# Kernel tuning notes

Hardware: AMD Instinct MI355X
Metric: run time of the kernel (lower is better)

Reference implementation:

```python
import jax, jax.numpy as jnp
import numpy as np

K = 20
EPS = 1e-5
DILATIONS = (1, 2, 4)


def _bn(x, g, b, m, v):
    # inference-mode BatchNorm1d (eval: running stats)
    return (x - m) / jnp.sqrt(v + EPS) * g + b


def _dilated_adj(x, dilation, k):
    B, N, _ = x.shape
    sq = jnp.sum(x * x, axis=-1)
    # squared pairwise distance: monotonic in p=2 cdist -> identical topk indices
    dist2 = sq[:, :, None] + sq[:, None, :] - 2.0 * jnp.einsum('bnc,bmc->bnm', x, x)
    dk = min(k * dilation, N - 1)
    _, idx = jax.lax.top_k(-dist2, dk + 1)          # smallest distances
    sampled = idx[:, :, 1::dilation][:, :, :k]      # skip self, dilated sample (B,N,k)
    bidx = jnp.arange(B)[:, None, None]
    ridx = jnp.arange(N)[None, :, None]
    return jnp.zeros((B, N, N), x.dtype).at[bidx, ridx, sampled].set(1.0)


def _normalize(adj):
    # add self loops then symmetric normalization D^-1/2 (A+I) D^-1/2
    N = adj.shape[1]
    a = adj + jnp.eye(N, dtype=adj.dtype)
    dinv = 1.0 / jnp.sqrt(jnp.sum(a, axis=2))       # degrees >= 1, no inf
    return dinv[:, :, None] * a * dinv[:, None, :]


def _gcn_layer(x, adj, W, b, g, bb, m, v):
    h = x @ W + b                                   # (B,N,Cout)
    h = jnp.einsum('bnm,bmc->bnc', adj, h)          # dense aggregation (bmm)
    return jax.nn.relu(_bn(h, g, bb, m, v))         # dropout is identity in eval


def _forward(x, Wg0, bg0, g0g, g0b, g0m, g0v, Wg1, bg1, g1g, g1b, g1m, g1v, Wg2, bg2, g2g, g2b, g2m, g2v, W1, b1, n1g, n1b, n1m, n1v, W2, b2, n2g, n2b, n2m, n2v, W3, b3, n3g, n3b, n3m, n3v, W4, b4, n4g, n4b, n4m, n4v, W5, b5, n5g, n5b, n5m, n5v, W6, b6):
    gcn_params = ((Wg0, bg0, g0g, g0b, g0m, g0v),
                  (Wg1, bg1, g1g, g1b, g1m, g1v),
                  (Wg2, bg2, g2g, g2b, g2m, g2v))
    feats = x
    ms = []
    for (W, b, g, bb, m, v), dil in zip(gcn_params, DILATIONS):
        adj = _normalize(_dilated_adj(feats, dil, K))
        feats = _gcn_layer(feats, adj, W, b, g, bb, m, v)
        ms.append(feats)
    f = jnp.stack(ms, axis=-1).mean(axis=-1)        # multi-scale mean (B,N,64)
    f = jax.nn.relu(_bn(f @ W1 + b1, n1g, n1b, n1m, n1v))
    f = jax.nn.relu(_bn(f @ W2 + b2, n2g, n2b, n2m, n2v))
    f = jax.nn.relu(_bn(f @ W3 + b3, n3g, n3b, n3m, n3v))
    f = jnp.max(f, axis=1)                          # MaxPool1d(N) over points -> (B,1024)
    f = jax.nn.relu(_bn(f @ W4 + b4, n4g, n4b, n4m, n4v))
    f = jax.nn.relu(_bn(f @ W5 + b5, n5g, n5b, n5m, n5v))
    return f @ W6 + b6                              # (B,40)


def setup_inputs():
    key = jax.random.key(0)
    ks = iter(jax.random.split(key, 32))
    d = {'x': jax.random.normal(next(ks), (32, 1024, 3), jnp.float32)}

    def lin(wn, bn_, ci, co):
        d[wn] = jax.random.normal(next(ks), (ci, co), jnp.float32) * 0.05
        d[bn_] = jnp.zeros((co,), jnp.float32)

    def bnp(p, c):
        d[p + 'g'] = jnp.ones((c,), jnp.float32)
        d[p + 'b'] = jnp.zeros((c,), jnp.float32)
        d[p + 'm'] = jnp.zeros((c,), jnp.float32)
        d[p + 'v'] = jnp.ones((c,), jnp.float32)

    for i, (ci, co) in enumerate(((3, 64), (64, 64), (64, 64))):
        lin('Wg%d' % i, 'bg%d' % i, ci, co)
        bnp('g%d' % i, co)
    for i, (ci, co) in enumerate(((64, 128), (128, 512), (512, 1024), (1024, 1024), (1024, 512)), start=1):
        lin('W%d' % i, 'b%d' % i, ci, co)
        bnp('n%d' % i, co)
    lin('W6', 'b6', 512, 40)
    return d


def reference(x, Wg0, bg0, g0g, g0b, g0m, g0v, Wg1, bg1, g1g, g1b, g1m, g1v, Wg2, bg2, g2g, g2b, g2m, g2v, W1, b1, n1g, n1b, n1m, n1v, W2, b2, n2g, n2b, n2m, n2v, W3, b3, n3g, n3b, n3m, n3v, W4, b4, n4g, n4b, n4m, n4v, W5, b5, n5g, n5b, n5m, n5v, W6, b6):
    return _forward(x, Wg0, bg0, g0g, g0b, g0m, g0v, Wg1, bg1, g1g, g1b, g1m, g1v, Wg2, bg2, g2g, g2b, g2m, g2v, W1, b1, n1g, n1b, n1m, n1v, W2, b2, n2g, n2b, n2m, n2v, W3, b3, n3g, n3b, n3m, n3v, W4, b4, n4g, n4b, n4m, n4v, W5, b5, n5g, n5b, n5m, n5v, W6, b6)
```

## Files before the change

kernel.cpp:

```cpp
#include <hip/hip_runtime.h>
#include <stdint.h>

#define KNN_K 20
#define EPSBN 1e-5f

typedef __attribute__((ext_vector_type(4))) float f32x4;
typedef __attribute__((ext_vector_type(8))) short s16x8;
typedef __attribute__((ext_vector_type(4))) short s16x4;

__device__ __forceinline__ unsigned sortable_f32(float f) {
    unsigned u = __float_as_uint(f);
    return (u & 0x80000000u) ? ~u : (u | 0x80000000u);
}

__device__ __forceinline__ short f2bf(float x) {
    unsigned u = __float_as_uint(x);
    unsigned r = (u + 0x7fffu + ((u >> 16) & 1u)) >> 16;
    return (short)r;
}
__device__ __forceinline__ float bf2f(short h) {
    return __uint_as_float(((unsigned)(unsigned short)h) << 16);
}

__global__ void sq_kernel(const float* __restrict__ x, float* __restrict__ sq,
                          int total, int C) {
    int i = blockIdx.x * 256 + threadIdx.x;
    if (i >= total) return;
    const float* p = x + (size_t)i * C;
    float s = 0.f;
    for (int c = 0; c < C; ++c) s += p[c] * p[c];
    sq[i] = s;
}

__global__ __launch_bounds__(256) void dist128_kernel(
    const float* __restrict__ feats, const float* __restrict__ sq,
    float* __restrict__ dist, int b0, int N, int C)
{
    int lb = blockIdx.z;
    int b = b0 + lb;
    const float* F = feats + (size_t)b * N * C;
    const float* S = sq + (size_t)b * N;
    float* D = dist + (size_t)lb * N * N;
    int n0 = blockIdx.y * 128, m0 = blockIdx.x * 128;
    __shared__ float As[16][132];
    __shared__ float Bs[16][132];
    int tx = threadIdx.x & 15, ty = threadIdx.x >> 4;
    int tid = threadIdx.x;
    float acc[8][8] = {};
    for (int k0 = 0; k0 < C; k0 += 16) {
        #pragma unroll
        for (int it = 0; it < 8; ++it) {
            int idx = tid + it * 256;
            int r = idx >> 4, kk = idx & 15;
            int gk = k0 + kk;
            As[kk][r] = (gk < C) ? F[(size_t)(n0 + r) * C + gk] : 0.f;
            Bs[kk][r] = (gk < C) ? F[(size_t)(m0 + r) * C + gk] : 0.f;
        }
        __syncthreads();
        #pragma unroll
        for (int kk = 0; kk < 16; ++kk) {
            float4 a0 = *reinterpret_cast<const float4*>(&As[kk][ty * 4]);
            float4 a1 = *reinterpret_cast<const float4*>(&As[kk][64 + ty * 4]);
            float4 b0 = *reinterpret_cast<const float4*>(&Bs[kk][tx * 4]);
            float4 b1 = *reinterpret_cast<const float4*>(&Bs[kk][64 + tx * 4]);
            float av[8] = {a0.x, a0.y, a0.z, a0.w, a1.x, a1.y, a1.z, a1.w};
            float bv[8] = {b0.x, b0.y, b0.z, b0.w, b1.x, b1.y, b1.z, b1.w};
            #pragma unroll
            for (int i = 0; i < 8; ++i)
                #pragma unroll
                for (int j = 0; j < 8; ++j)
                    acc[i][j] = fmaf(av[i], bv[j], acc[i][j]);
        }
        __syncthreads();
    }
    #pragma unroll
    for (int i = 0; i < 8; ++i) {
        int n = n0 + ((i < 4) ? ty * 4 + i : 64 + ty * 4 + (i - 4));
        float sn = S[n];
        #pragma unroll
        for (int j = 0; j < 8; ++j) {
            int m = m0 + ((j < 4) ? tx * 4 + j : 64 + tx * 4 + (j - 4));
            D[(size_t)n * N + m] = (sn + S[m]) - 2.0f * acc[i][j];
        }
    }
}

__global__ __launch_bounds__(256) void knn_agg_kernel(
    const float* __restrict__ dist, const float* __restrict__ lin,
    const float* __restrict__ gam, const float* __restrict__ bet,
    const float* __restrict__ mu, const float* __restrict__ var,
    float* __restrict__ feats_out, float* __restrict__ ms,
    short* __restrict__ msh, short* __restrict__ msl,
    int b0, int N, int dil, int mode)
{
    __shared__ unsigned long long keys[1024];
    __shared__ unsigned hist[2048];
    __shared__ unsigned long long cand[256];
    __shared__ int nbrs[KNN_K];
    __shared__ float aggP[4][64];
    __shared__ int wsum[4];
    __shared__ int svC0, svP, svD, svCounter;

    int t = threadIdx.x;
    int lb = blockIdx.x / N;
    int n = blockIdx.x - lb * N;
    int b = b0 + lb;
    const int R = KNN_K * dil + 1;

    const float* drow = dist + ((size_t)lb * N + n) * N;
    unsigned long long myk[4];
    #pragma unroll
    for (int s = 0; s < 4; ++s) {
        int m = t + 256 * s;
        float dv = drow[m];
        myk[s] = ((unsigned long long)sortable_f32(dv) << 32) | (unsigned)m;
        keys[m] = myk[s];
    }
    #pragma unroll
    for (int h = 0; h < 8; ++h) hist[t * 8 + h] = 0u;
    if (t == 0) svCounter = 0;
    __syncthreads();
    #pragma unroll
    for (int s = 0; s < 4; ++s)
        atomicAdd(&hist[(unsigned)(myk[s] >> 53)], 1u);
    __syncthreads();
    int psum = 0;
    #pragma unroll
    for (int h = 0; h < 8; ++h) psum += (int)hist[t * 8 + h];
    int lane = t & 63, wv = t >> 6;
    int val = psum;
    #pragma unroll
    for (int d = 1; d < 64; d <<= 1) {
        int o = __shfl_up(val, d, 64);
        if (lane >= d) val += o;
    }
    if (lane == 63) wsum[wv] = val;
    __syncthreads();
    int prefix = 0;
    for (int i = 0; i < wv; ++i) prefix += wsum[i];
    int incl = val + prefix;
    int excl = incl - psum;
    if (excl < R && incl >= R) {
        int cum = excl;
        for (int h = 0; h < 8; ++h) {
            int hv = (int)hist[t * 8 + h];
            if (cum + hv >= R) { svD = t * 8 + h; svC0 = cum; svP = hv; break; }
            cum += hv;
        }
    }
    __syncthreads();
    int Cnt = svC0 + svP;
    if (Cnt <= 256) {
        unsigned dpiv = (unsigned)svD;
        #pragma unroll
        for (int s = 0; s < 4; ++s) {
            if ((unsigned)(myk[s] >> 53) <= dpiv) {
                int pos = atomicAdd(&svCounter, 1);
                cand[pos] = myk[s];
            }
        }
        __syncthreads();
        if (t < Cnt) {
            unsigned long long my = cand[t];
            int r = 0;
            for (int c = 0; c < Cnt; ++c) r += (cand[c] < my) ? 1 : 0;
            if (r >= 1) {
                int q = r - 1;
                if (q % dil == 0) {
                    int j = q / dil;
                    if (j < KNN_K) nbrs[j] = (int)(my & 0xFFFFFFFFull);
                }
            }
        }
        __syncthreads();
    } else {
        for (int kk = 2; kk <= 1024; kk <<= 1) {
            for (int jj = kk >> 1; jj > 0; jj >>= 1) {
                __syncthreads();
                #pragma unroll
                for (int s = 0; s < 4; ++s) {
                    int i = t + 256 * s;
                    int ixj = i ^ jj;
                    if (ixj > i) {
                        unsigned long long a = keys[i], c = keys[ixj];
                        bool up = ((i & kk) == 0);
                        if ((a > c) == up) { keys[i] = c; keys[ixj] = a; }
                    }
                }
            }
        }
        __syncthreads();
        if (t < KNN_K) nbrs[t] = (int)(keys[1 + t * dil] & 0xFFFFFFFFull);
        __syncthreads();
    }
    {
        int c = t & 63, g = t >> 6;
        float pacc = 0.f;
        for (int j = g; j < KNN_K; j += 4)
            pacc += lin[((size_t)b * N + nbrs[j]) * 64 + c];
        aggP[g][c] = pacc;
    }
    __syncthreads();
    if (t < 64) {
        const float sc = 1.0f / 21.0f;
        size_t base = ((size_t)b * N + n) * 64;
        float acc = lin[base + t] + aggP[0][t] + aggP[1][t] + aggP[2][t] + aggP[3][t];
        float v = acc * sc;
        v = (v - mu[t]) / sqrtf(var[t] + EPSBN) * gam[t] + bet[t];
        v = fmaxf(v, 0.f);
        if (feats_out) feats_out[base + t] = v;
        if (mode == 0) ms[base + t] = v;
        else if (mode == 1) ms[base + t] += v;
        else {
            float m3 = (ms[base + t] + v) * (1.0f / 3.0f);
            short hh = f2bf(m3);
            msh[base + t] = hh;
            msl[base + t] = f2bf(m3 - bf2f(hh));
        }
    }
}

template<int EPI>
__global__ __launch_bounds__(256) void gemm_kernel(
    const float* __restrict__ A, const float* __restrict__ W,
    const float* __restrict__ bias,
    const float* __restrict__ gam, const float* __restrict__ bet,
    const float* __restrict__ mu, const float* __restrict__ var,
    float* __restrict__ C,
    int M, int K, int N)
{
    __shared__ float As[16][68];
    __shared__ float Bs[16][68];
    int tx = threadIdx.x, ty = threadIdx.y;
    int tid = ty * 16 + tx;
    int row0 = blockIdx.y * 64, col0 = blockIdx.x * 64;
    float acc[4][4] = {};
    for (int k0 = 0; k0 < K; k0 += 16) {
        #pragma unroll
        for (int it = 0; it < 4; ++it) {
            int idx = tid + it * 256;
            int r = idx >> 4, kk = idx & 15;
            int gr = row0 + r, gk = k0 + kk;
            As[kk][r] = (gr < M && gk < K) ? A[(size_t)gr * K + gk] : 0.f;
        }
        #pragma unroll
        for (int it = 0; it < 4; ++it) {
            int idx = tid + it * 256;
            int kk = idx >> 6, c = idx & 63;
            int gk = k0 + kk, gc = col0 + c;
            Bs[kk][c] = (gk < K && gc < N) ? W[(size_t)gk * N + gc] : 0.f;
        }
        __syncthreads();
        #pragma unroll
        for (int kk = 0; kk < 16; ++kk) {
            float4 a4 = *reinterpret_cast<const float4*>(&As[kk][ty * 4]);
            float4 b4 = *reinterpret_cast<const float4*>(&Bs[kk][tx * 4]);
            float av[4] = {a4.x, a4.y, a4.z, a4.w};
            float bv[4] = {b4.x, b4.y, b4.z, b4.w};
            #pragma unroll
            for (int i = 0; i < 4; ++i)
                #pragma unroll
                for (int j = 0; j < 4; ++j)
                    acc[i][j] = fmaf(av[i], bv[j], acc[i][j]);
        }
        __syncthreads();
    }
    #pragma unroll
    for (int i = 0; i < 4; ++i) {
        int r = row0 + ty * 4 + i;
        if (r >= M) break;
        #pragma unroll
        for (int j = 0; j < 4; ++j) {
            int c = col0 + tx * 4 + j;
            if (c >= N) continue;
            float val = acc[i][j] + bias[c];
            if (EPI >= 1) {
                val = (val - mu[c]) / sqrtf(var[c] + EPSBN) * gam[c] + bet[c];
                val = fmaxf(val, 0.f);
            }
            C[(size_t)r * N + c] = val;
        }
    }
}

__global__ __launch_bounds__(256) void skinny_gemm_kernel(
    const float* __restrict__ A, const float* __restrict__ W,
    float* __restrict__ part, int K, int N)
{
    __shared__ float Alds[32][260];
    int tid = threadIdx.x;
    int col0 = blockIdx.x * 32;
    int kc = blockIdx.y;
    int k0 = kc * 256;
    #pragma unroll
    for (int it = 0; it < 8; ++it) {
        int idx = tid + it * 256;
        int r = idx >> 6, kq = (idx & 63) * 4;
        f32x4 v = *(const f32x4*)&A[(size_t)r * K + k0 + kq];
        *(f32x4*)&Alds[r][kq] = v;
    }
    __syncthreads();

    int col = col0 + (tid & 31);
    int g = tid >> 5;
    bool colok = col < N;
    const float* Wp = W + (size_t)k0 * N + (colok ? col : 0);
    float acc0 = 0.f, acc1 = 0.f, acc2 = 0.f, acc3 = 0.f;
    #pragma unroll 4
    for (int k = 0; k < 256; ++k) {
        float wv = Wp[(size_t)k * N];
        acc0 = fmaf(Alds[g * 4 + 0][k], wv, acc0);
        acc1 = fmaf(Alds[g * 4 + 1][k], wv, acc1);
        acc2 = fmaf(Alds[g * 4 + 2][k], wv, acc2);
        acc3 = fmaf(Alds[g * 4 + 3][k], wv, acc3);
    }
    if (colok) {
        size_t base = ((size_t)kc * 32 + g * 4) * N + col;
        part[base]         = acc0;
        part[base + N]     = acc1;
        part[base + 2 * N] = acc2;
        part[base + 3 * N] = acc3;
    }
}

template<int EPI>
__global__ void skinny_reduce_kernel(
    const float* __restrict__ part, const float* __restrict__ bias,
    const float* __restrict__ gam, const float* __restrict__ bet,
    const float* __restrict__ mu, const float* __restrict__ var,
    float* __restrict__ C, int M, int N, int kchunks)
{
    int i = blockIdx.x * 256 + threadIdx.x;
    if (i >= M * N) return;
    int c = i % N;
    float s = 0.f;
    for (int kc = 0; kc < kchunks; ++kc) s += part[(size_t)kc * M * N + i];
    float val = s + bias[c];
    if (EPI >= 1) {
        val = (val - mu[c]) / sqrtf(var[c] + EPSBN) * gam[c] + bet[c];
        val = fmaxf(val, 0.f);
    }
    C[i] = val;
}

__global__ void split_wt_kernel(const float* __restrict__ W,
                                short* __restrict__ Bh, short* __restrict__ Bl,
                                int K, int N)
{
    int n = blockIdx.x * 64 + threadIdx.x;
    if (n >= N) return;
    for (int k0 = 0; k0 < K; k0 += 8) {
        s16x8 h, l;
        #pragma unroll
        for (int e = 0; e < 8; ++e) {
            float x = W[(size_t)(k0 + e) * N + n];
            short hh = f2bf(x);
            h[e] = hh;
            l[e] = f2bf(x - bf2f(hh));
        }
        *(s16x8*)&Bh[(size_t)n * K + k0] = h;
        *(s16x8*)&Bl[(size_t)n * K + k0] = l;
    }
}

template<int EPI>
__global__ __launch_bounds__(256) void gemm_mfma_kernel(
    const short* __restrict__ Ah, const short* __restrict__ Al,
    const short* __restrict__ Bh, const short* __restrict__ Bl,
    const float* __restrict__ bias,
    const float* __restrict__ gam, const float* __restrict__ bet,
    const float* __restrict__ mu, const float* __restrict__ var,
    short* __restrict__ Chi, short* __restrict__ Clo,
    float* __restrict__ pool,
    int M, int K, int N, int rowsPerBatch)
{
    __shared__ short Alds[128][72];
    __shared__ short Blds[128][72];
    __shared__ int poolS[128];

    int tid = threadIdx.x;
    int wave = tid >> 6, lane = tid & 63;
    int wr = wave >> 1, wc = wave & 1;
    int row0 = blockIdx.y * 128, col0 = blockIdx.x * 128;
    int fr = lane & 15, fq = lane >> 4;
    int kb = fq * 8;

    f32x4 acc[4][4] = {};

    for (int k0 = 0; k0 < K; k0 += 32) {
        #pragma unroll
        for (int it = 0; it < 2; ++it) {
            int idx = tid + it * 256;
            int r = idx >> 2, ch = (idx & 3) * 8;
            size_t go = (size_t)(row0 + r) * K + k0 + ch;
            *(s16x8*)&Alds[r][ch]      = *(const s16x8*)&Ah[go];
            *(s16x8*)&Alds[r][32 + ch] = *(const s16x8*)&Al[go];
        }
        #pragma unroll
        for (int it = 0; it < 2; ++it) {
            int idx = tid + it * 256;
            int c = idx >> 2, ch = (idx & 3) * 8;
            size_t bo = (size_t)(col0 + c) * K + k0 + ch;
            *(s16x8*)&Blds[c][ch]      = *(const s16x8*)&Bh[bo];
            *(s16x8*)&Blds[c][32 + ch] = *(const s16x8*)&Bl[bo];
        }
        __syncthreads();

        s16x8 ah[4], al[4], bhf[4], blf[4];
        #pragma unroll
        for (int i = 0; i < 4; ++i) {
            int r = wr * 64 + i * 16 + fr;
            ah[i] = *(const s16x8*)&Alds[r][kb];
            al[i] = *(const s16x8*)&Alds[r][32 + kb];
        }
        #pragma unroll
        for (int j = 0; j < 4; ++j) {
            int c = wc * 64 + j * 16 + fr;
            bhf[j] = *(const s16x8*)&Blds[c][kb];
            blf[j] = *(const s16x8*)&Blds[c][32 + kb];
        }
        #pragma unroll
        for (int i = 0; i < 4; ++i)
            #pragma unroll
            for (int j = 0; j < 4; ++j) {
                acc[i][j] = __builtin_amdgcn_mfma_f32_16x16x32_bf16(ah[i], bhf[j], acc[i][j], 0, 0, 0);
                acc[i][j] = __builtin_amdgcn_mfma_f32_16x16x32_bf16(ah[i], blf[j], acc[i][j], 0, 0, 0);
                acc[i][j] = __builtin_amdgcn_mfma_f32_16x16x32_bf16(al[i], bhf[j], acc[i][j], 0, 0, 0);
            }
        __syncthreads();
    }

    if (EPI == 1) {
        #pragma unroll
        for (int j = 0; j < 4; ++j) {
            int col = col0 + wc * 64 + j * 16 + fr;
            float bs = bias[col], g = gam[col], be = bet[col], m = mu[col];
            float inv = 1.0f / sqrtf(var[col] + EPSBN);
            #pragma unroll
            for (int i = 0; i < 4; ++i) {
                int rbase = row0 + wr * 64 + i * 16 + fq * 4;
                #pragma unroll
                for (int reg = 0; reg < 4; ++reg) {
                    float val = acc[i][j][reg] + bs;
                    val = (val - m) * inv * g + be;
                    val = fmaxf(val, 0.f);
                    short hh = f2bf(val);
                    size_t o = (size_t)(rbase + reg) * N + col;
                    Chi[o] = hh;
                    Clo[o] = f2bf(val - bf2f(hh));
                }
            }
        }
    } else {
        float cmax[4];
        #pragma unroll
        for (int j = 0; j < 4; ++j) {
            int col = col0 + wc * 64 + j * 16 + fr;
            float bs = bias[col], g = gam[col], be = bet[col], m = mu[col];
            float inv = 1.0f / sqrtf(var[col] + EPSBN);
            float cm = 0.f;
            #pragma unroll
            for (int i = 0; i < 4; ++i)
                #pragma unroll
                for (int reg = 0; reg < 4; ++reg) {
                    float val = acc[i][j][reg] + bs;
                    val = (val - m) * inv * g + be;
                    val = fmaxf(val, 0.f);
                    cm = fmaxf(cm, val);
                }
            cmax[j] = cm;
        }
        #pragma unroll
        for (int j = 0; j < 4; ++j) {
            cmax[j] = fmaxf(cmax[j], __shfl_xor(cmax[j], 16, 64));
            cmax[j] = fmaxf(cmax[j], __shfl_xor(cmax[j], 32, 64));
        }
        if (tid < 128) poolS[tid] = 0;
        __syncthreads();
        if (fq == 0) {
            #pragma unroll
            for (int j = 0; j < 4; ++j)
                atomicMax(&poolS[wc * 64 + j * 16 + fr], __float_as_int(cmax[j]));
        }
        __syncthreads();
        if (tid < 128) {
            int bb = row0 / rowsPerBatch;
            atomicMax((int*)&pool[(size_t)bb * N + col0 + tid], poolS[tid]);
        }
    }
}

extern "C" void kernel_launch(void* const* d_in, const int* in_sizes, int n_in,
                              void* d_out, int out_size, void* d_ws, size_t ws_size,
                              hipStream_t stream)
{
    (void)in_sizes; (void)n_in; (void)out_size;
    const int B = 32, N = 1024, MBN = B * N;
    const float* x = (const float*)d_in[0];

    const float *Wg[3], *bg[3], *gg[3], *gb[3], *gm[3], *gv[3];
    for (int i = 0; i < 3; ++i) {
        int base = 1 + i * 6;
        Wg[i] = (const float*)d_in[base + 0];
        bg[i] = (const float*)d_in[base + 1];
        gg[i] = (const float*)d_in[base + 2];
        gb[i] = (const float*)d_in[base + 3];
        gm[i] = (const float*)d_in[base + 4];
        gv[i] = (const float*)d_in[base + 5];
    }
    const float *Wm[5], *bm[5], *ng[5], *nb[5], *nm[5], *nv[5];
    for (int i = 0; i < 5; ++i) {
        int base = 19 + i * 6;
        Wm[i] = (const float*)d_in[base + 0];
        bm[i] = (const float*)d_in[base + 1];
        ng[i] = (const float*)d_in[base + 2];
        nb[i] = (const float*)d_in[base + 3];
        nm[i] = (const float*)d_in[base + 4];
        nv[i] = (const float*)d_in[base + 5];
    }
    const float* W6 = (const float*)d_in[49];
    const float* b6 = (const float*)d_in[50];

    char* w = (char*)d_ws;
    size_t off = 0;
    auto allocB = [&](size_t bytes) {
        void* p = w + off;
        off += (bytes + 255) & ~(size_t)255;
        return p;
    };
    float* ms     = (float*)allocB((size_t)MBN * 64 * 4);
    float* fA     = (float*)allocB((size_t)MBN * 64 * 4);
    float* fB     = (float*)allocB((size_t)MBN * 64 * 4);
    float* lin    = (float*)allocB((size_t)MBN * 64 * 4);
    float* sqv    = (float*)allocB((size_t)MBN * 4);
    float* pooled = (float*)allocB((size_t)B * 1024 * 4);
    float* f4     = (float*)allocB((size_t)B * 1024 * 4);
    float* f5     = (float*)allocB((size_t)B * 512 * 4);
    float* skpart = (float*)allocB((size_t)4 * 32 * 1024 * 4);
    short* msh    = (short*)allocB((size_t)MBN * 64 * 2);
    short* msl    = (short*)allocB((size_t)MBN * 64 * 2);
    short* w1h    = (short*)allocB((size_t)64 * 128 * 2);
    short* w1l    = (short*)allocB((size_t)64 * 128 * 2);
    short* w2h    = (short*)allocB((size_t)128 * 512 * 2);
    short* w2l    = (short*)allocB((size_t)128 * 512 * 2);
    short* w3h    = (short*)allocB((size_t)512 * 1024 * 2);
    short* w3l    = (short*)allocB((size_t)512 * 1024 * 2);
    size_t bigOff = off;
    short* f1h = (short*)(w + bigOff);
    short* f1l = (short*)(w + bigOff + 1 * (size_t)MBN * 128 * 2);
    short* f2h = (short*)(w + bigOff + 2 * (size_t)MBN * 128 * 2);
    short* f2l = (short*)(w + bigOff + 2 * (size_t)MBN * 128 * 2 + (size_t)MBN * 512 * 2);
    float* distB = (float*)(w + bigOff);
    size_t distBytes = (size_t)N * N * sizeof(float);
    int chunkB = 1;
    if (ws_size > bigOff) {
        size_t cap = (ws_size - bigOff) / distBytes;
        chunkB = (int)(cap < 32 ? cap : 32);
        if (chunkB < 1) chunkB = 1;
    }

    dim3 blk16(16, 16);
    auto grid64  = [](int M, int Nn) { return dim3((unsigned)((Nn + 63) / 64), (unsigned)((M + 63) / 64)); };
    auto gridMf  = [](int M, int Nn) { return dim3((unsigned)(Nn / 128), (unsigned)(M / 128)); };

    split_wt_kernel<<<dim3(128 / 64), 64, 0, stream>>>(Wm[0], w1h, w1l, 64, 128);
    split_wt_kernel<<<dim3(512 / 64), 64, 0, stream>>>(Wm[1], w2h, w2l, 128, 512);
    split_wt_kernel<<<dim3(1024 / 64), 64, 0, stream>>>(Wm[2], w3h, w3l, 512, 1024);

    const float* featsIn = x;
    float* featsOutArr[3] = { fA, fB, nullptr };
    int Cin[3] = { 3, 64, 64 };
    int dils[3] = { 1, 2, 4 };
    for (int L = 0; L < 3; ++L) {
        sq_kernel<<<(MBN + 255) / 256, 256, 0, stream>>>(featsIn, sqv, MBN, Cin[L]);
        gemm_kernel<0><<<grid64(MBN, 64), blk16, 0, stream>>>(
            featsIn, Wg[L], bg[L], nullptr, nullptr, nullptr, nullptr,
            lin, MBN, Cin[L], 64);
        for (int b0 = 0; b0 < B; b0 += chunkB) {
            int cb = (B - b0 < chunkB) ? (B - b0) : chunkB;
            dist128_kernel<<<dim3(8, 8, (unsigned)cb), 256, 0, stream>>>(
                featsIn, sqv, distB, b0, N, Cin[L]);
            knn_agg_kernel<<<cb * N, 256, 0, stream>>>(
                distB, lin, gg[L], gb[L], gm[L], gv[L],
                featsOutArr[L], ms, msh, msl, b0, N, dils[L], L);
        }
        featsIn = featsOutArr[L];
    }

    gemm_mfma_kernel<1><<<gridMf(MBN, 128), 256, 0, stream>>>(
        msh, msl, w1h, w1l, bm[0], ng[0], nb[0], nm[0], nv[0],
        f1h, f1l, nullptr, MBN, 64, 128, N);
    gemm_mfma_kernel<1><<<gridMf(MBN, 512), 256, 0, stream>>>(
        f1h, f1l, w2h, w2l, bm[1], ng[1], nb[1], nm[1], nv[1],
        f2h, f2l, nullptr, MBN, 128, 512, N);
    hipMemsetAsync(pooled, 0, (size_t)B * 1024 * sizeof(float), stream);
    gemm_mfma_kernel<2><<<gridMf(MBN, 1024), 256, 0, stream>>>(
        f2h, f2l, w3h, w3l, bm[2], ng[2], nb[2], nm[2], nv[2],
        nullptr, nullptr, pooled, MBN, 512, 1024, N);

    skinny_gemm_kernel<<<dim3(1024 / 32, 4), 256, 0, stream>>>(pooled, Wm[3], skpart, 1024, 1024);
    skinny_reduce_kernel<1><<<(32 * 1024 + 255) / 256, 256, 0, stream>>>(
        skpart, bm[3], ng[3], nb[3], nm[3], nv[3], f4, 32, 1024, 4);
    skinny_gemm_kernel<<<dim3(512 / 32, 4), 256, 0, stream>>>(f4, Wm[4], skpart, 1024, 512);
    skinny_reduce_kernel<1><<<(32 * 512 + 255) / 256, 256, 0, stream>>>(
        skpart, bm[4], ng[4], nb[4], nm[4], nv[4], f5, 32, 512, 4);
    skinny_gemm_kernel<<<dim3(2, 2), 256, 0, stream>>>(f5, W6, skpart, 512, 40);
    skinny_reduce_kernel<0><<<(32 * 40 + 255) / 256, 256, 0, stream>>>(
        skpart, b6, nullptr, nullptr, nullptr, nullptr, (float*)d_out, 32, 40, 2);
}
```

Baseline: 817.2 us.

## Exploit distance symmetry, alias sort keys onto histogram LDS, XCD-aware GEMM tile mapping

The distance kernel now computes only upper-triangular 128x128 tiles (36 instead of 64) and writes each off-diagonal tile twice, once transposed, so the pairwise GEMM work is roughly halved. The kNN kernel drops its separate 8 KB keys array and reuses the histogram LDS for the bitonic-sort fallback, cutting shared memory per block to allow higher occupancy. The MFMA GEMMs switch to a 1D grid that maps blocks to tiles per XCD, aiming for better L2 locality across MI355X chiplets. The transposed writes are strided and uncoalesced, and the remap assumes the row-tile count divides by 8.

```diff
diff --git a/kernel.cpp b/kernel.cpp
--- a/kernel.cpp
+++ b/kernel.cpp
@@ -32,7 +32,7 @@
     sq[i] = s;
 }
 
-__global__ __launch_bounds__(256) void dist128_kernel(
+__global__ __launch_bounds__(256) void dist128t_kernel(
     const float* __restrict__ feats, const float* __restrict__ sq,
     float* __restrict__ dist, int b0, int N, int C)
 {
@@ -41,7 +41,11 @@
     const float* F = feats + (size_t)b * N * C;
     const float* S = sq + (size_t)b * N;
     float* D = dist + (size_t)lb * N * N;
-    int n0 = blockIdx.y * 128, m0 = blockIdx.x * 128;
+    int t = blockIdx.x, bi = 0;
+    while (t >= 8 - bi) { t -= 8 - bi; ++bi; }
+    int bj = bi + t;
+    int n0 = bi * 128, m0 = bj * 128;
+
     __shared__ float As[16][132];
     __shared__ float Bs[16][132];
     int tx = threadIdx.x & 15, ty = threadIdx.x >> 4;
@@ -83,6 +87,18 @@
             D[(size_t)n * N + m] = (sn + S[m]) - 2.0f * acc[i][j];
         }
     }
+    if (bi < bj) {
+        #pragma unroll
+        for (int j = 0; j < 8; ++j) {
+            int m = m0 + ((j < 4) ? tx * 4 + j : 64 + tx * 4 + (j - 4));
+            float sm = S[m];
+            #pragma unroll
+            for (int i = 0; i < 8; ++i) {
+                int n = n0 + ((i < 4) ? ty * 4 + i : 64 + ty * 4 + (i - 4));
+                D[(size_t)m * N + n] = (sm + S[n]) - 2.0f * acc[i][j];
+            }
+        }
+    }
 }
 
 __global__ __launch_bounds__(256) void knn_agg_kernel(
@@ -93,8 +109,7 @@
     short* __restrict__ msh, short* __restrict__ msl,
     int b0, int N, int dil, int mode)
 {
-    __shared__ unsigned long long keys[1024];
-    __shared__ unsigned hist[2048];
+    __shared__ alignas(16) unsigned hist[2048];
     __shared__ unsigned long long cand[256];
     __shared__ int nbrs[KNN_K];
     __shared__ float aggP[4][64];
@@ -114,7 +129,6 @@
         int m = t + 256 * s;
         float dv = drow[m];
         myk[s] = ((unsigned long long)sortable_f32(dv) << 32) | (unsigned)m;
-        keys[m] = myk[s];
     }
     #pragma unroll
     for (int h = 0; h < 8; ++h) hist[t * 8 + h] = 0u;
@@ -174,6 +188,9 @@
         }
         __syncthreads();
     } else {
+        unsigned long long* keys = (unsigned long long*)hist;
+        #pragma unroll
+        for (int s = 0; s < 4; ++s) keys[t + 256 * s] = myk[s];
         for (int kk = 2; kk <= 1024; kk <<= 1) {
             for (int jj = kk >> 1; jj > 0; jj >>= 1) {
                 __syncthreads();
@@ -381,7 +398,14 @@
     int tid = threadIdx.x;
     int wave = tid >> 6, lane = tid & 63;
     int wr = wave >> 1, wc = wave & 1;
-    int row0 = blockIdx.y * 128, col0 = blockIdx.x * 128;
+    int nx = N >> 7;
+    int rowsPerXcd = (M >> 7) >> 3;
+    int bid = blockIdx.x;
+    int xcd = bid & 7, l = bid >> 3;
+    int tileY = xcd * rowsPerXcd + l / nx;
+    int tileX = l - (l / nx) * nx;
+    int row0 = tileY * 128, col0 = tileX * 128;
+
     int fr = lane & 15, fq = lane >> 4;
     int kb = fq * 8;
 
@@ -561,7 +585,7 @@
 
     dim3 blk16(16, 16);
     auto grid64  = [](int M, int Nn) { return dim3((unsigned)((Nn + 63) / 64), (unsigned)((M + 63) / 64)); };
-    auto gridMf  = [](int M, int Nn) { return dim3((unsigned)(Nn / 128), (unsigned)(M / 128)); };
+    auto gridMf1 = [](int M, int Nn) { return dim3((unsigned)((Nn / 128) * (M / 128))); };
 
     split_wt_kernel<<<dim3(128 / 64), 64, 0, stream>>>(Wm[0], w1h, w1l, 64, 128);
     split_wt_kernel<<<dim3(512 / 64), 64, 0, stream>>>(Wm[1], w2h, w2l, 128, 512);
@@ -578,7 +602,7 @@
             lin, MBN, Cin[L], 64);
         for (int b0 = 0; b0 < B; b0 += chunkB) {
             int cb = (B - b0 < chunkB) ? (B - b0) : chunkB;
-            dist128_kernel<<<dim3(8, 8, (unsigned)cb), 256, 0, stream>>>(
+            dist128t_kernel<<<dim3(36, 1, (unsigned)cb), 256, 0, stream>>>(
                 featsIn, sqv, distB, b0, N, Cin[L]);
             knn_agg_kernel<<<cb * N, 256, 0, stream>>>(
                 distB, lin, gg[L], gb[L], gm[L], gv[L],
@@ -587,14 +611,14 @@
         featsIn = featsOutArr[L];
     }
 
-    gemm_mfma_kernel<1><<<gridMf(MBN, 128), 256, 0, stream>>>(
+    gemm_mfma_kernel<1><<<gridMf1(MBN, 128), 256, 0, stream>>>(
         msh, msl, w1h, w1l, bm[0], ng[0], nb[0], nm[0], nv[0],
         f1h, f1l, nullptr, MBN, 64, 128, N);
-    gemm_mfma_kernel<1><<<gridMf(MBN, 512), 256, 0, stream>>>(
+    gemm_mfma_kernel<1><<<gridMf1(MBN, 512), 256, 0, stream>>>(
         f1h, f1l, w2h, w2l, bm[1], ng[1], nb[1], nm[1], nv[1],
         f2h, f2l, nullptr, MBN, 128, 512, N);
     hipMemsetAsync(pooled, 0, (size_t)B * 1024 * sizeof(float), stream);
-    gemm_mfma_kernel<2><<<gridMf(MBN, 1024), 256, 0, stream>>>(
+    gemm_mfma_kernel<2><<<gridMf1(MBN, 1024), 256, 0, stream>>>(
         f2h, f2l, w3h, w3l, bm[2], ng[2], nb[2], nm[2], nv[2],
         nullptr, nullptr, pooled, MBN, 512, 1024, N);
 
```

New measurement: 761.1 us. -6.9%, faster.
